# Performance work log

Hardware: AMD Instinct MI355X
Metric: run time of the kernel (lower is better)

Reference implementation:

```python
import jax, jax.numpy as jnp
import numpy as np

L = 12        # depth
DIM = 768     # model dim
HEADS = 12
DHEAD = 64
INNER = HEADS * DHEAD   # 768
MLP = 3072
P = 16        # patch size
IMG = 384
C = 3
B = 16
NCLS = 1000
NPATCH = (IMG // P) ** 2   # 576
N = NPATCH + 1             # 577 (cls token)
PATCH_DIM = C * P * P      # 768
SCALE = DIM ** (-0.5)      # NOTE: original scales by dim, not dim_head


def setup_inputs() -> dict:
    key = jax.random.key(0)
    ks = jax.random.split(key, 21)
    rn = lambda k, shape, s=0.02: jax.random.normal(k, shape, dtype=jnp.float32) * s
    return {
        "img": jax.random.normal(ks[0], (B, C, IMG, IMG), dtype=jnp.float32),
        "patch_w": rn(ks[1], (PATCH_DIM, DIM)),
        "patch_b": rn(ks[2], (DIM,)),
        "pos_emb": rn(ks[3], (1, N, DIM), 1.0),
        "cls_tok": rn(ks[4], (1, 1, DIM), 1.0),
        "ln1_w": jnp.ones((L, DIM), jnp.float32),
        "ln1_b": jnp.zeros((L, DIM), jnp.float32),
        "qkv_w": rn(ks[5], (L, DIM, 3 * INNER)),
        "out_w": rn(ks[6], (L, INNER, DIM)),
        "out_b": rn(ks[7], (L, DIM)),
        "ln2_w": jnp.ones((L, DIM), jnp.float32),
        "ln2_b": jnp.zeros((L, DIM), jnp.float32),
        "ff1_w": rn(ks[8], (L, DIM, MLP)),
        "ff1_b": rn(ks[9], (L, MLP)),
        "ff2_w": rn(ks[10], (L, MLP, DIM)),
        "ff2_b": rn(ks[11], (L, DIM)),
        "head_ln_w": jnp.ones((DIM,), jnp.float32),
        "head_ln_b": jnp.zeros((DIM,), jnp.float32),
        "head_w": rn(ks[12], (DIM, NCLS)),
        "head_b": rn(ks[13], (NCLS,)),
    }


def layer_norm(x, w, b, eps=1e-5):
    mu = jnp.mean(x, axis=-1, keepdims=True)
    var = jnp.mean(jnp.square(x - mu), axis=-1, keepdims=True)
    return (x - mu) * jax.lax.rsqrt(var + eps) * w + b


def _vit_forward(img, patch_w, patch_b, pos_emb, cls_tok,
                 ln1_w, ln1_b, qkv_w, out_w, out_b,
                 ln2_w, ln2_b, ff1_w, ff1_b, ff2_w, ff2_b,
                 head_ln_w, head_ln_b, head_w, head_b):
    b = img.shape[0]
    g = IMG // P
    # rearrange 'b c (h p1) (w p2) -> b (h w) (p1 p2 c)'
    x = img.reshape(b, C, g, P, g, P).transpose(0, 2, 4, 3, 5, 1).reshape(b, NPATCH, PATCH_DIM)
    x = x @ patch_w + patch_b                           # [b, 576, dim]
    cls = jnp.broadcast_to(cls_tok, (b, 1, DIM))
    x = jnp.concatenate([cls, x], axis=1) + pos_emb[:, :N]   # [b, 577, dim]

    def block(x, p):
        l1w, l1b, qkvw, ow, ob, l2w, l2b, f1w, f1b, f2w, f2b = p
        # attention (pre-norm, residual inside Attention.forward)
        h = layer_norm(x, l1w, l1b)
        qkv = h @ qkvw                                  # [b, n, 3*inner]
        q, k, v = jnp.split(qkv, 3, axis=-1)
        to_heads = lambda t: t.reshape(b, N, HEADS, DHEAD).transpose(0, 2, 1, 3)
        q, k, v = to_heads(q), to_heads(k), to_heads(v)  # [b, h, n, d]
        dots = jnp.einsum('bhid,bhjd->bhij', q, k) * SCALE
        attn = jax.nn.softmax(dots, axis=-1)
        o = jnp.einsum('bhij,bhjd->bhid', attn, v)
        o = o.transpose(0, 2, 1, 3).reshape(b, N, INNER)
        x = x + (o @ ow + ob)
        # feedforward (pre-norm, residual)
        h2 = layer_norm(x, l2w, l2b)
        h2 = jax.nn.gelu(h2 @ f1w + f1b, approximate=False)
        x = x + (h2 @ f2w + f2b)
        return x, None

    x, _ = jax.lax.scan(block, x,
                        (ln1_w, ln1_b, qkv_w, out_w, out_b,
                         ln2_w, ln2_b, ff1_w, ff1_b, ff2_w, ff2_b))
    cls_out = x[:, 0]                                   # [b, dim]
    return layer_norm(cls_out, head_ln_w, head_ln_b) @ head_w + head_b


def reference(img, patch_w, patch_b, pos_emb, cls_tok,
              ln1_w, ln1_b, qkv_w, out_w, out_b,
              ln2_w, ln2_b, ff1_w, ff1_b, ff2_w, ff2_b,
              head_ln_w, head_ln_b, head_w, head_b):
    return _vit_forward(img, patch_w, patch_b, pos_emb, cls_tok,
                        ln1_w, ln1_b, qkv_w, out_w, out_b,
                        ln2_w, ln2_b, ff1_w, ff1_b, ff2_w, ff2_b,
                        head_ln_w, head_ln_b, head_w, head_b)
```

## Files before the change

### kernel.cpp

```cpp
#include <hip/hip_runtime.h>
#include <cstdint>


typedef __attribute__((ext_vector_type(8))) short bf16x8;
typedef __attribute__((ext_vector_type(4))) float f32x4;

#define NTOK 577

__device__ __forceinline__ ushort f2bf(float f) {
  union { float f; unsigned int u; } x; x.f = f;
  unsigned int r = x.u + 0x7fffu + ((x.u >> 16) & 1u);
  return (ushort)(r >> 16);
}

__device__ __forceinline__ void gload_lds16(const ushort* g, ushort* l) {
  __builtin_amdgcn_global_load_lds(
      (const __attribute__((address_space(1))) unsigned int*)g,
      (__attribute__((address_space(3))) unsigned int*)l, 16, 0, 0);
}

#define VMCNT0 asm volatile("s_waitcnt vmcnt(0)" ::: "memory")
#define LGKM0  asm volatile("s_waitcnt lgkmcnt(0)" ::: "memory")
#define SCHED0 __builtin_amdgcn_sched_barrier(0)
#define BARRIER __builtin_amdgcn_s_barrier()

__device__ __forceinline__ int gsw(int row) {
  return (row & 7) + 2 * ((row >> 4) & 3);
}

__global__ __launch_bounds__(256) void convt_kernel(const float* __restrict__ W,
                                                    ushort* __restrict__ Wt,
                                                    int K, int N) {
  __shared__ float t[32][33];
  const int kb = blockIdx.x * 32, nb = blockIdx.y * 32;
  const int tx = threadIdx.x & 31, ty = threadIdx.x >> 5;
#pragma unroll
  for (int i = 0; i < 32; i += 8)
    t[ty + i][tx] = W[(size_t)(kb + ty + i) * N + (nb + tx)];
  __syncthreads();
#pragma unroll
  for (int i = 0; i < 32; i += 8)
    Wt[(size_t)(nb + ty + i) * K + (kb + tx)] = f2bf(t[tx][ty + i]);
}

__global__ __launch_bounds__(256) void im2col_kernel(const float* __restrict__ img,
                                                     ushort* __restrict__ Ap) {
  const int idx = blockIdx.x * 256 + threadIdx.x;
  const int j = idx % 768;
  const int m = idx / 768;
  const int c = j % 3;
  const int q = j / 3;
  const int px = q & 15, py = q >> 4;
  const int b = m / 576, p = m % 576;
  const int gy = p / 24, gx = p % 24;
  const float v = img[((size_t)(b * 3 + c) * 384 + (gy * 16 + py)) * 384 + (gx * 16 + px)];
  Ap[idx] = f2bf(v);
}

__global__ void clspos_kernel(const float* __restrict__ cls_tok,
                              const float* __restrict__ pos,
                              float* __restrict__ x) {
  const int i = blockIdx.x * 256 + threadIdx.x;
  const int b = i / 768, d = i % 768;
  x[(size_t)b * NTOK * 768 + d] = cls_tok[d] + pos[d];
}

__global__ __launch_bounds__(64) void ln_kernel(const float* __restrict__ x,
                                                const float* __restrict__ w,
                                                const float* __restrict__ bb,
                                                ushort* __restrict__ out) {
  const int row = blockIdx.x, lane = threadIdx.x;
  const float4* xr = reinterpret_cast<const float4*>(x + (size_t)row * 768);
  const float4 v0 = xr[lane], v1 = xr[lane + 64], v2 = xr[lane + 128];
  float vals[12] = {v0.x, v0.y, v0.z, v0.w, v1.x, v1.y, v1.z, v1.w,
                    v2.x, v2.y, v2.z, v2.w};
  float s = 0.f;
#pragma unroll
  for (int i = 0; i < 12; ++i) s += vals[i];
#pragma unroll
  for (int o = 32; o; o >>= 1) s += __shfl_xor(s, o);
  const float mu = s * (1.0f / 768.0f);
  float q = 0.f;
#pragma unroll
  for (int i = 0; i < 12; ++i) { const float d = vals[i] - mu; q += d * d; }
#pragma unroll
  for (int o = 32; o; o >>= 1) q += __shfl_xor(q, o);
  const float rstd = rsqrtf(q * (1.0f / 768.0f) + 1e-5f);
  const float4* w4 = reinterpret_cast<const float4*>(w);
  const float4* b4 = reinterpret_cast<const float4*>(bb);
  ushort* orow = out + (size_t)row * 768;
#pragma unroll
  for (int ch = 0; ch < 3; ++ch) {
    const float4 wv = w4[lane + ch * 64];
    const float4 bv = b4[lane + ch * 64];
    ushort4 u;
    u.x = f2bf((vals[ch * 4 + 0] - mu) * rstd * wv.x + bv.x);
    u.y = f2bf((vals[ch * 4 + 1] - mu) * rstd * wv.y + bv.y);
    u.z = f2bf((vals[ch * 4 + 2] - mu) * rstd * wv.z + bv.z);
    u.w = f2bf((vals[ch * 4 + 3] - mu) * rstd * wv.w + bv.w);
    *reinterpret_cast<ushort4*>(orow + ch * 256 + lane * 4) = u;
  }
}

constexpr int EPI_BF16 = 0;
constexpr int EPI_GELU_BF16 = 1;
constexpr int EPI_RES_F32 = 2;
constexpr int EPI_PATCH = 3;

template <int EPI>
__global__ __launch_bounds__(256) void gemmP_kernel(
    const ushort* __restrict__ A, const ushort* __restrict__ Bt,
    const float* __restrict__ bias, const float* __restrict__ extra,
    void* __restrict__ Cptr, int M, int N, int K, int mt) {
  __shared__ ushort ldsA[2][128 * 64];
  __shared__ ushort ldsB[2][128 * 64];

  const int nwg = gridDim.x;
  const int orig = blockIdx.x;
  const int q8 = nwg >> 3, r8 = nwg & 7, xcd = orig & 7, sidx = orig >> 3;
  const int wg = (xcd < r8 ? xcd * (q8 + 1) : r8 * (q8 + 1) + (xcd - r8) * q8) + sidx;
  const int tileM = (wg % mt) * 128;
  const int tileN = (wg / mt) * 128;

  const int tid = threadIdx.x;
  const int wave = tid >> 6, lane = tid & 63;
  const int wm = wave >> 1, wn = wave & 1;
  const int lr = lane & 15, lg = lane >> 4;

  f32x4 acc[4][4];
#pragma unroll
  for (int m = 0; m < 4; ++m)
#pragma unroll
    for (int n = 0; n < 4; ++n) acc[m][n] = (f32x4){0.f, 0.f, 0.f, 0.f};

  const ushort* pA[4];
  const ushort* pB[4];
  int dst[4];
#pragma unroll
  for (int i = 0; i < 4; ++i) {
    const int c = wave * 4 + i;
    const int rowst = c * 8;
    dst[i] = rowst * 64;
    const int row = rowst + (lane >> 3);
    const int lgr = ((lane & 7) - gsw(row)) & 7;
    pA[i] = A + (size_t)(tileM + row) * K + lgr * 8;
    pB[i] = Bt + (size_t)(tileN + row) * K + lgr * 8;
  }

#define PSTAGE(buf, kk)                              \
  _Pragma("unroll") for (int i = 0; i < 4; ++i)      \
      gload_lds16(pA[i] + (kk), &ldsA[buf][dst[i]]); \
  _Pragma("unroll") for (int i = 0; i < 4; ++i)      \
      gload_lds16(pB[i] + (kk), &ldsB[buf][dst[i]]);

  PSTAGE(0, 0);

  const int NT = K >> 6;
  int cb = 0;
  for (int t = 0; t < NT; ++t) {
    VMCNT0; SCHED0;
    BARRIER;
    if (t + 1 < NT) { PSTAGE(cb ^ 1, (t + 1) * 64); }
    bf16x8 a[8], b[8];
#pragma unroll
    for (int mf = 0; mf < 4; ++mf) {
      const int row = wm * 64 + mf * 16 + lr;
#pragma unroll
      for (int ks = 0; ks < 2; ++ks) {
        const int pg = (ks * 4 + lg + (lr & 7) + 2 * mf) & 7;
        a[mf * 2 + ks] = *reinterpret_cast<const bf16x8*>(&ldsA[cb][row * 64 + pg * 8]);
      }
    }
#pragma unroll
    for (int nf = 0; nf < 4; ++nf) {
      const int row = wn * 64 + nf * 16 + lr;
#pragma unroll
      for (int ks = 0; ks < 2; ++ks) {
        const int pg = (ks * 4 + lg + (lr & 7) + 2 * nf) & 7;
        b[nf * 2 + ks] = *reinterpret_cast<const bf16x8*>(&ldsB[cb][row * 64 + pg * 8]);
      }
    }
    LGKM0; SCHED0;
    __builtin_amdgcn_s_setprio(1);
#pragma unroll
    for (int mf = 0; mf < 4; ++mf)
#pragma unroll
      for (int nf = 0; nf < 4; ++nf)
#pragma unroll
        for (int ks = 0; ks < 2; ++ks)
          acc[mf][nf] = __builtin_amdgcn_mfma_f32_16x16x32_bf16(
              a[mf * 2 + ks], b[nf * 2 + ks], acc[mf][nf], 0, 0, 0);
    __builtin_amdgcn_s_setprio(0);
    cb ^= 1;
  }

#pragma unroll
  for (int mf = 0; mf < 4; ++mf) {
#pragma unroll
    for (int r = 0; r < 4; ++r) {
      const int row = tileM + wm * 64 + mf * 16 + lg * 4 + r;
      if (row >= M) continue;
#pragma unroll
      for (int nf = 0; nf < 4; ++nf) {
        const int col = tileN + wn * 64 + nf * 16 + lr;
        float v = acc[mf][nf][r];
        if constexpr (EPI == EPI_BF16) {
          reinterpret_cast<ushort*>(Cptr)[(size_t)row * N + col] = f2bf(v);
        } else if constexpr (EPI == EPI_GELU_BF16) {
          v += bias[col];
          v = 0.5f * v * (1.0f + erff(v * 0.70710678118654752440f));
          reinterpret_cast<ushort*>(Cptr)[(size_t)row * N + col] = f2bf(v);
        } else if constexpr (EPI == EPI_RES_F32) {
          v += bias[col] + extra[(size_t)row * N + col];
          reinterpret_cast<float*>(Cptr)[(size_t)row * N + col] = v;
        } else {
          const int bb = row / 576;
          const int p = row - bb * 576;
          v += bias[col] + extra[(size_t)(p + 1) * 768 + col];
          reinterpret_cast<float*>(Cptr)[(size_t)(row + bb + 1) * 768 + col] = v;
        }
      }
    }
  }
#undef PSTAGE
}

__global__ __launch_bounds__(256) void attn_kernel(const ushort* __restrict__ qkv,
                                                   ushort* __restrict__ o) {
  __shared__ ushort sK[64 * 64];
  __shared__ ushort sVt[64 * 64];
  __shared__ ushort sP[4][16 * 72];
  const int bh = blockIdx.x;
  const int b = bh / 12, hh = bh % 12;
  const int q0 = blockIdx.y * 64;
  const int tid = threadIdx.x;
  const int wave = tid >> 6, lane = tid & 63;
  const int lr = lane & 15;
  const int lg = lane >> 4;
  const ushort* base = qkv + (size_t)b * NTOK * 2304 + hh * 64;
  const float SC = 0.03608439182435161f;

  bf16x8 qf[2];
  {
    const int qrow = q0 + wave * 16 + lr;
    if (qrow < NTOK) {
      const ushort* qp = base + (size_t)qrow * 2304 + lg * 8;
      qf[0] = *reinterpret_cast<const bf16x8*>(qp);
      qf[1] = *reinterpret_cast<const bf16x8*>(qp + 32);
    } else {
      qf[0] = (bf16x8){0, 0, 0, 0, 0, 0, 0, 0};
      qf[1] = qf[0];
    }
  }

  float mst[4], lst[4];
  f32x4 oacc[4];
#pragma unroll
  for (int i = 0; i < 4; ++i) {
    mst[i] = -1e30f; lst[i] = 0.f;
    oacc[i] = (f32x4){0.f, 0.f, 0.f, 0.f};
  }

  const int skey = tid >> 2;
  const int sc4 = tid & 3;
  const int gswk = gsw(skey);

  for (int t0 = 0; t0 < NTOK; t0 += 64) {
    __syncthreads();
    {
      const int gk = t0 + skey;
      int4 k0v, k1v, v0v, v1v;
      if (gk < NTOK) {
        const int4* kp = reinterpret_cast<const int4*>(base + (size_t)gk * 2304 + 768 + sc4 * 16);
        k0v = kp[0]; k1v = kp[1];
        const int4* vp = reinterpret_cast<const int4*>(base + (size_t)gk * 2304 + 1536 + sc4 * 16);
        v0v = vp[0]; v1v = vp[1];
      } else {
        int4 z; z.x = z.y = z.z = z.w = 0;
        k0v = k1v = v0v = v1v = z;
      }
      *reinterpret_cast<int4*>(&sK[skey * 64 + (((2 * sc4 + 0) + gswk) & 7) * 8]) = k0v;
      *reinterpret_cast<int4*>(&sK[skey * 64 + (((2 * sc4 + 1) + gswk) & 7) * 8]) = k1v;
      const ushort* vs = reinterpret_cast<const ushort*>(&v0v);
      const ushort* vs2 = reinterpret_cast<const ushort*>(&v1v);
#pragma unroll
      for (int i = 0; i < 8; ++i) {
        const int d0 = sc4 * 16 + i;
        const int pg0 = ((skey >> 3) + gsw(d0)) & 7;
        sVt[d0 * 64 + pg0 * 8 + (skey & 7)] = vs[i];
        const int d1 = sc4 * 16 + 8 + i;
        const int pg1 = ((skey >> 3) + gsw(d1)) & 7;
        sVt[d1 * 64 + pg1 * 8 + (skey & 7)] = vs2[i];
      }
    }
    __syncthreads();

    f32x4 sacc[4];
#pragma unroll
    for (int n = 0; n < 4; ++n) sacc[n] = (f32x4){0.f, 0.f, 0.f, 0.f};
#pragma unroll
    for (int n = 0; n < 4; ++n) {
      const int row = n * 16 + lr;
      const int rot = (lr & 7) + 2 * n;
      const bf16x8 kf0 = *reinterpret_cast<const bf16x8*>(&sK[row * 64 + ((lg + rot) & 7) * 8]);
      const bf16x8 kf1 = *reinterpret_cast<const bf16x8*>(&sK[row * 64 + ((4 + lg + rot) & 7) * 8]);
      sacc[n] = __builtin_amdgcn_mfma_f32_16x16x32_bf16(qf[0], kf0, sacc[n], 0, 0, 0);
      sacc[n] = __builtin_amdgcn_mfma_f32_16x16x32_bf16(qf[1], kf1, sacc[n], 0, 0, 0);
    }

    float s[4][4], pm[4];
#pragma unroll
    for (int reg = 0; reg < 4; ++reg) pm[reg] = -1e30f;
#pragma unroll
    for (int n = 0; n < 4; ++n)
#pragma unroll
      for (int reg = 0; reg < 4; ++reg) {
        float v = sacc[n][reg] * SC;
        if (t0 + n * 16 + lr >= NTOK) v = -1e30f;
        s[n][reg] = v;
        pm[reg] = fmaxf(pm[reg], v);
      }
#pragma unroll
    for (int off = 1; off < 16; off <<= 1)
#pragma unroll
      for (int reg = 0; reg < 4; ++reg) pm[reg] = fmaxf(pm[reg], __shfl_xor(pm[reg], off));

    float al[4], rs[4];
#pragma unroll
    for (int reg = 0; reg < 4; ++reg) {
      const float mn = fmaxf(mst[reg], pm[reg]);
      al[reg] = __expf(mst[reg] - mn);
      mst[reg] = mn;
      rs[reg] = 0.f;
    }
#pragma unroll
    for (int n = 0; n < 4; ++n)
#pragma unroll
      for (int reg = 0; reg < 4; ++reg) {
        s[n][reg] = __expf(s[n][reg] - mst[reg]);
        rs[reg] += s[n][reg];
      }
#pragma unroll
    for (int off = 1; off < 16; off <<= 1)
#pragma unroll
      for (int reg = 0; reg < 4; ++reg) rs[reg] += __shfl_xor(rs[reg], off);
#pragma unroll
    for (int reg = 0; reg < 4; ++reg) {
      lst[reg] = lst[reg] * al[reg] + rs[reg];
#pragma unroll
      for (int n = 0; n < 4; ++n) oacc[n][reg] *= al[reg];
    }

#pragma unroll
    for (int n = 0; n < 4; ++n)
#pragma unroll
      for (int reg = 0; reg < 4; ++reg)
        sP[wave][(lg * 4 + reg) * 72 + n * 16 + lr] = f2bf(s[n][reg]);

    const bf16x8 pf0 = *reinterpret_cast<const bf16x8*>(&sP[wave][lr * 72 + lg * 8]);
    const bf16x8 pf1 = *reinterpret_cast<const bf16x8*>(&sP[wave][lr * 72 + 32 + lg * 8]);
#pragma unroll
    for (int n = 0; n < 4; ++n) {
      const int row = n * 16 + lr;
      const int rot = (lr & 7) + 2 * n;
      const bf16x8 vf0 = *reinterpret_cast<const bf16x8*>(&sVt[row * 64 + ((lg + rot) & 7) * 8]);
      const bf16x8 vf1 = *reinterpret_cast<const bf16x8*>(&sVt[row * 64 + ((4 + lg + rot) & 7) * 8]);
      oacc[n] = __builtin_amdgcn_mfma_f32_16x16x32_bf16(pf0, vf0, oacc[n], 0, 0, 0);
      oacc[n] = __builtin_amdgcn_mfma_f32_16x16x32_bf16(pf1, vf1, oacc[n], 0, 0, 0);
    }
  }

#pragma unroll
  for (int reg = 0; reg < 4; ++reg) {
    const int q = q0 + wave * 16 + lg * 4 + reg;
    if (q >= NTOK) continue;
    const float inv = 1.0f / lst[reg];
    ushort* op = o + (size_t)(b * NTOK + q) * 768 + hh * 64;
#pragma unroll
    for (int n = 0; n < 4; ++n) op[n * 16 + lr] = f2bf(oacc[n][reg] * inv);
  }
}

__global__ __launch_bounds__(256) void head_kernel(const float* __restrict__ x,
                                                   const float* __restrict__ lw,
                                                   const float* __restrict__ lb,
                                                   const float* __restrict__ hw,
                                                   const float* __restrict__ hb,
                                                   float* __restrict__ out) {
  __shared__ float srow[768];
  __shared__ float sred[8];
  const int b = blockIdx.x, tid = threadIdx.x;
  const float* xr = x + (size_t)b * NTOK * 768;
  for (int i = tid; i < 768; i += 256) srow[i] = xr[i];
  __syncthreads();
  float part = srow[tid] + srow[tid + 256] + srow[tid + 512];
#pragma unroll
  for (int off = 32; off; off >>= 1) part += __shfl_xor(part, off);
  if ((tid & 63) == 0) sred[tid >> 6] = part;
  __syncthreads();
  const float mu = (sred[0] + sred[1] + sred[2] + sred[3]) * (1.0f / 768.0f);
  const float d0 = srow[tid] - mu, d1 = srow[tid + 256] - mu, d2 = srow[tid + 512] - mu;
  float vp = d0 * d0 + d1 * d1 + d2 * d2;
#pragma unroll
  for (int off = 32; off; off >>= 1) vp += __shfl_xor(vp, off);
  if ((tid & 63) == 0) sred[4 + (tid >> 6)] = vp;
  __syncthreads();
  const float rstd = rsqrtf((sred[4] + sred[5] + sred[6] + sred[7]) * (1.0f / 768.0f) + 1e-5f);
  for (int i = tid; i < 768; i += 256) srow[i] = (srow[i] - mu) * rstd * lw[i] + lb[i];
  __syncthreads();
  const int c = blockIdx.y * 250 + tid;
  if (tid < 250 && c < 1000) {
    float a = 0.f;
#pragma unroll 4
    for (int k = 0; k < 768; ++k) a += srow[k] * hw[(size_t)k * 1000 + c];
    out[b * 1000 + c] = a + hb[c];
  }
}

extern "C" void kernel_launch(void* const* d_in, const int* in_sizes, int n_in,
                              void* d_out, int out_size, void* d_ws, size_t ws_size,
                              hipStream_t stream) {
  const float* img     = (const float*)d_in[0];
  const float* patch_w = (const float*)d_in[1];
  const float* patch_b = (const float*)d_in[2];
  const float* pos_emb = (const float*)d_in[3];
  const float* cls_tok = (const float*)d_in[4];
  const float* ln1_w   = (const float*)d_in[5];
  const float* ln1_b   = (const float*)d_in[6];
  const float* qkv_w   = (const float*)d_in[7];
  const float* out_w   = (const float*)d_in[8];
  const float* out_b   = (const float*)d_in[9];
  const float* ln2_w   = (const float*)d_in[10];
  const float* ln2_b   = (const float*)d_in[11];
  const float* ff1_w   = (const float*)d_in[12];
  const float* ff1_b   = (const float*)d_in[13];
  const float* ff2_w   = (const float*)d_in[14];
  const float* ff2_b   = (const float*)d_in[15];
  const float* hln_w   = (const float*)d_in[16];
  const float* hln_b   = (const float*)d_in[17];
  const float* head_w  = (const float*)d_in[18];
  const float* head_b  = (const float*)d_in[19];
  float* outp = (float*)d_out;

  char* wsp = (char*)d_ws;
  auto alloc = [&](size_t bytes) {
    char* p = wsp;
    wsp += (bytes + 255) & ~(size_t)255;
    return p;
  };
  float*  x    = (float*) alloc((size_t)9232 * 768 * 4);
  ushort* h    = (ushort*)alloc((size_t)9232 * 768 * 2);
  ushort* qkvb = (ushort*)alloc((size_t)9232 * 2304 * 2);
  ushort* mlp  = (ushort*)alloc((size_t)9232 * 3072 * 2);
  ushort* wq   = (ushort*)alloc((size_t)768 * 2304 * 2);
  ushort* wo   = (ushort*)alloc((size_t)768 * 768 * 2);
  ushort* w1   = (ushort*)alloc((size_t)768 * 3072 * 2);
  ushort* w2   = (ushort*)alloc((size_t)3072 * 768 * 2);
  ushort* apatch = mlp;
  ushort* wpatch = wq;

  convt_kernel<<<dim3(24, 24), 256, 0, stream>>>(patch_w, wpatch, 768, 768);
  im2col_kernel<<<27648, 256, 0, stream>>>(img, apatch);
  gemmP_kernel<EPI_PATCH><<<72 * 6, 256, 0, stream>>>(
      apatch, wpatch, patch_b, pos_emb, x, 9216, 768, 768, 72);
  clspos_kernel<<<48, 256, 0, stream>>>(cls_tok, pos_emb, x);

  for (int l = 0; l < 12; ++l) {
    ln_kernel<<<9232, 64, 0, stream>>>(x, ln1_w + l * 768, ln1_b + l * 768, h);
    convt_kernel<<<dim3(24, 72), 256, 0, stream>>>(qkv_w + (size_t)l * 768 * 2304, wq, 768, 2304);
    gemmP_kernel<EPI_BF16><<<73 * 18, 256, 0, stream>>>(
        h, wq, nullptr, nullptr, qkvb, 9232, 2304, 768, 73);
    attn_kernel<<<dim3(192, 10), 256, 0, stream>>>(qkvb, h);
    convt_kernel<<<dim3(24, 24), 256, 0, stream>>>(out_w + (size_t)l * 768 * 768, wo, 768, 768);
    gemmP_kernel<EPI_RES_F32><<<73 * 6, 256, 0, stream>>>(
        h, wo, out_b + l * 768, x, x, 9232, 768, 768, 73);
    ln_kernel<<<9232, 64, 0, stream>>>(x, ln2_w + l * 768, ln2_b + l * 768, h);
    convt_kernel<<<dim3(24, 96), 256, 0, stream>>>(ff1_w + (size_t)l * 768 * 3072, w1, 768, 3072);
    gemmP_kernel<EPI_GELU_BF16><<<73 * 24, 256, 0, stream>>>(
        h, w1, ff1_b + l * 3072, nullptr, mlp, 9232, 3072, 768, 73);
    convt_kernel<<<dim3(96, 24), 256, 0, stream>>>(ff2_w + (size_t)l * 3072 * 768, w2, 3072, 768);
    gemmP_kernel<EPI_RES_F32><<<73 * 6, 256, 0, stream>>>(
        mlp, w2, ff2_b + l * 768, x, x, 9232, 768, 3072, 73);
  }

  head_kernel<<<dim3(16, 4), 256, 0, stream>>>(x, hln_w, hln_b, head_w, head_b, outp);
}
```

Before: 4.485 ms.

## Batch weight conversions, pack LN rows, prefetch attention KV, reorder GEMM tiles

Merges the four per-layer weight transpose/convert launches into one kernel, so there is one launch per layer instead of four. LayerNorm now processes four rows per 256-thread block instead of one row per 64-thread block. Attention software-prefetches the next K/V tile into registers while the current tile is computed. The QKV and FF1 GEMMs switch to N-fastest tile ordering, which may improve L2 reuse of A tiles. The head kernel splits K across waves and uses more blocks.

```diff
diff --git a/kernel.cpp b/kernel.cpp
--- a/kernel.cpp
+++ b/kernel.cpp
@@ -28,19 +28,47 @@
   return (row & 7) + 2 * ((row >> 4) & 3);
 }
 
+__device__ __forceinline__ void transpose_tile(const float* __restrict__ W,
+                                               ushort* __restrict__ Wt,
+                                               int K, int N, int kb, int nb,
+                                               int tx, int ty, float t[32][33]) {
+#pragma unroll
+  for (int i = 0; i < 32; i += 8)
+    t[ty + i][tx] = W[(size_t)(kb + ty + i) * N + (nb + tx)];
+  __syncthreads();
+#pragma unroll
+  for (int i = 0; i < 32; i += 8)
+    Wt[(size_t)(nb + ty + i) * K + (kb + tx)] = f2bf(t[tx][ty + i]);
+}
+
 __global__ __launch_bounds__(256) void convt_kernel(const float* __restrict__ W,
                                                     ushort* __restrict__ Wt,
                                                     int K, int N) {
   __shared__ float t[32][33];
-  const int kb = blockIdx.x * 32, nb = blockIdx.y * 32;
+  transpose_tile(W, Wt, K, N, blockIdx.x * 32, blockIdx.y * 32,
+                 threadIdx.x & 31, threadIdx.x >> 5, t);
+}
+
+__global__ __launch_bounds__(256) void wconv_kernel(
+    const float* __restrict__ qkv_w, const float* __restrict__ out_w,
+    const float* __restrict__ ff1_w, const float* __restrict__ ff2_w,
+    ushort* __restrict__ wq, ushort* __restrict__ wo,
+    ushort* __restrict__ w1, ushort* __restrict__ w2) {
+  __shared__ float t[32][33];
   const int tx = threadIdx.x & 31, ty = threadIdx.x >> 5;
-#pragma unroll
-  for (int i = 0; i < 32; i += 8)
-    t[ty + i][tx] = W[(size_t)(kb + ty + i) * N + (nb + tx)];
-  __syncthreads();
-#pragma unroll
-  for (int i = 0; i < 32; i += 8)
-    Wt[(size_t)(nb + ty + i) * K + (kb + tx)] = f2bf(t[tx][ty + i]);
+  int bx = blockIdx.x;
+  if (bx < 1728) {
+    transpose_tile(qkv_w, wq, 768, 2304, (bx % 24) * 32, (bx / 24) * 32, tx, ty, t);
+  } else if (bx < 2304) {
+    bx -= 1728;
+    transpose_tile(out_w, wo, 768, 768, (bx % 24) * 32, (bx / 24) * 32, tx, ty, t);
+  } else if (bx < 4608) {
+    bx -= 2304;
+    transpose_tile(ff1_w, w1, 768, 3072, (bx % 24) * 32, (bx / 24) * 32, tx, ty, t);
+  } else {
+    bx -= 4608;
+    transpose_tile(ff2_w, w2, 3072, 768, (bx % 96) * 32, (bx / 96) * 32, tx, ty, t);
+  }
 }
 
 __global__ __launch_bounds__(256) void im2col_kernel(const float* __restrict__ img,
@@ -65,11 +93,12 @@
   x[(size_t)b * NTOK * 768 + d] = cls_tok[d] + pos[d];
 }
 
-__global__ __launch_bounds__(64) void ln_kernel(const float* __restrict__ x,
-                                                const float* __restrict__ w,
-                                                const float* __restrict__ bb,
-                                                ushort* __restrict__ out) {
-  const int row = blockIdx.x, lane = threadIdx.x;
+__global__ __launch_bounds__(256) void ln_kernel(const float* __restrict__ x,
+                                                 const float* __restrict__ w,
+                                                 const float* __restrict__ bb,
+                                                 ushort* __restrict__ out) {
+  const int wave = threadIdx.x >> 6, lane = threadIdx.x & 63;
+  const int row = blockIdx.x * 4 + wave;
   const float4* xr = reinterpret_cast<const float4*>(x + (size_t)row * 768);
   const float4 v0 = xr[lane], v1 = xr[lane + 64], v2 = xr[lane + 128];
   float vals[12] = {v0.x, v0.y, v0.z, v0.w, v1.x, v1.y, v1.z, v1.w,
@@ -107,7 +136,7 @@
 constexpr int EPI_RES_F32 = 2;
 constexpr int EPI_PATCH = 3;
 
-template <int EPI>
+template <int EPI, bool NFAST>
 __global__ __launch_bounds__(256) void gemmP_kernel(
     const ushort* __restrict__ A, const ushort* __restrict__ Bt,
     const float* __restrict__ bias, const float* __restrict__ extra,
@@ -119,8 +148,14 @@
   const int orig = blockIdx.x;
   const int q8 = nwg >> 3, r8 = nwg & 7, xcd = orig & 7, sidx = orig >> 3;
   const int wg = (xcd < r8 ? xcd * (q8 + 1) : r8 * (q8 + 1) + (xcd - r8) * q8) + sidx;
-  const int tileM = (wg % mt) * 128;
-  const int tileN = (wg / mt) * 128;
+  int tileM, tileN;
+  if (NFAST) {
+    tileM = (wg / mt) * 128;
+    tileN = (wg % mt) * 128;
+  } else {
+    tileM = (wg % mt) * 128;
+    tileN = (wg / mt) * 128;
+  }
 
   const int tid = threadIdx.x;
   const int wave = tid >> 6, lane = tid & 63;
@@ -265,20 +300,24 @@
   const int sc4 = tid & 3;
   const int gswk = gsw(skey);
 
+  int4 k0v, k1v, v0v, v1v;
+  auto load_kv = [&](int t0) {
+    const int gk = t0 + skey;
+    if (gk < NTOK) {
+      const int4* kp = reinterpret_cast<const int4*>(base + (size_t)gk * 2304 + 768 + sc4 * 16);
+      k0v = kp[0]; k1v = kp[1];
+      const int4* vp = reinterpret_cast<const int4*>(base + (size_t)gk * 2304 + 1536 + sc4 * 16);
+      v0v = vp[0]; v1v = vp[1];
+    } else {
+      int4 z; z.x = z.y = z.z = z.w = 0;
+      k0v = k1v = v0v = v1v = z;
+    }
+  };
+  load_kv(0);
+
   for (int t0 = 0; t0 < NTOK; t0 += 64) {
     __syncthreads();
     {
-      const int gk = t0 + skey;
-      int4 k0v, k1v, v0v, v1v;
-      if (gk < NTOK) {
-        const int4* kp = reinterpret_cast<const int4*>(base + (size_t)gk * 2304 + 768 + sc4 * 16);
-        k0v = kp[0]; k1v = kp[1];
-        const int4* vp = reinterpret_cast<const int4*>(base + (size_t)gk * 2304 + 1536 + sc4 * 16);
-        v0v = vp[0]; v1v = vp[1];
-      } else {
-        int4 z; z.x = z.y = z.z = z.w = 0;
-        k0v = k1v = v0v = v1v = z;
-      }
       *reinterpret_cast<int4*>(&sK[skey * 64 + (((2 * sc4 + 0) + gswk) & 7) * 8]) = k0v;
       *reinterpret_cast<int4*>(&sK[skey * 64 + (((2 * sc4 + 1) + gswk) & 7) * 8]) = k1v;
       const ushort* vs = reinterpret_cast<const ushort*>(&v0v);
@@ -295,6 +334,8 @@
     }
     __syncthreads();
 
+    if (t0 + 64 < NTOK) load_kv(t0 + 64);
+
     f32x4 sacc[4];
 #pragma unroll
     for (int n = 0; n < 4; ++n) sacc[n] = (f32x4){0.f, 0.f, 0.f, 0.f};
@@ -389,7 +430,8 @@
                                                    float* __restrict__ out) {
   __shared__ float srow[768];
   __shared__ float sred[8];
-  const int b = blockIdx.x, tid = threadIdx.x;
+  __shared__ float spart[4][64];
+  const int b = blockIdx.x, ct = blockIdx.y, tid = threadIdx.x;
   const float* xr = x + (size_t)b * NTOK * 768;
   for (int i = tid; i < 768; i += 256) srow[i] = xr[i];
   __syncthreads();
@@ -408,12 +450,21 @@
   const float rstd = rsqrtf((sred[4] + sred[5] + sred[6] + sred[7]) * (1.0f / 768.0f) + 1e-5f);
   for (int i = tid; i < 768; i += 256) srow[i] = (srow[i] - mu) * rstd * lw[i] + lb[i];
   __syncthreads();
-  const int c = blockIdx.y * 250 + tid;
-  if (tid < 250 && c < 1000) {
-    float a = 0.f;
-#pragma unroll 4
-    for (int k = 0; k < 768; ++k) a += srow[k] * hw[(size_t)k * 1000 + c];
-    out[b * 1000 + c] = a + hb[c];
+  const int cl = tid & 63, kq = tid >> 6;
+  const int c = ct * 64 + cl;
+  float a = 0.f;
+  if (c < 1000) {
+    const int k0 = kq * 192;
+#pragma unroll 8
+    for (int k = k0; k < k0 + 192; ++k) a += srow[k] * hw[(size_t)k * 1000 + c];
+  }
+  spart[kq][cl] = a;
+  __syncthreads();
+  if (tid < 64) {
+    const int c2 = ct * 64 + tid;
+    if (c2 < 1000)
+      out[b * 1000 + c2] =
+          spart[0][tid] + spart[1][tid] + spart[2][tid] + spart[3][tid] + hb[c2];
   }
 }
 
@@ -461,27 +512,27 @@
 
   convt_kernel<<<dim3(24, 24), 256, 0, stream>>>(patch_w, wpatch, 768, 768);
   im2col_kernel<<<27648, 256, 0, stream>>>(img, apatch);
-  gemmP_kernel<EPI_PATCH><<<72 * 6, 256, 0, stream>>>(
+  gemmP_kernel<EPI_PATCH, false><<<72 * 6, 256, 0, stream>>>(
       apatch, wpatch, patch_b, pos_emb, x, 9216, 768, 768, 72);
   clspos_kernel<<<48, 256, 0, stream>>>(cls_tok, pos_emb, x);
 
   for (int l = 0; l < 12; ++l) {
-    ln_kernel<<<9232, 64, 0, stream>>>(x, ln1_w + l * 768, ln1_b + l * 768, h);
-    convt_kernel<<<dim3(24, 72), 256, 0, stream>>>(qkv_w + (size_t)l * 768 * 2304, wq, 768, 2304);
-    gemmP_kernel<EPI_BF16><<<73 * 18, 256, 0, stream>>>(
-        h, wq, nullptr, nullptr, qkvb, 9232, 2304, 768, 73);
+    wconv_kernel<<<6912, 256, 0, stream>>>(
+        qkv_w + (size_t)l * 768 * 2304, out_w + (size_t)l * 768 * 768,
+        ff1_w + (size_t)l * 768 * 3072, ff2_w + (size_t)l * 3072 * 768,
+        wq, wo, w1, w2);
+    ln_kernel<<<2308, 256, 0, stream>>>(x, ln1_w + l * 768, ln1_b + l * 768, h);
+    gemmP_kernel<EPI_BF16, true><<<73 * 18, 256, 0, stream>>>(
+        h, wq, nullptr, nullptr, qkvb, 9232, 2304, 768, 18);
     attn_kernel<<<dim3(192, 10), 256, 0, stream>>>(qkvb, h);
-    convt_kernel<<<dim3(24, 24), 256, 0, stream>>>(out_w + (size_t)l * 768 * 768, wo, 768, 768);
-    gemmP_kernel<EPI_RES_F32><<<73 * 6, 256, 0, stream>>>(
+    gemmP_kernel<EPI_RES_F32, false><<<73 * 6, 256, 0, stream>>>(
         h, wo, out_b + l * 768, x, x, 9232, 768, 768, 73);
-    ln_kernel<<<9232, 64, 0, stream>>>(x, ln2_w + l * 768, ln2_b + l * 768, h);
-    convt_kernel<<<dim3(24, 96), 256, 0, stream>>>(ff1_w + (size_t)l * 768 * 3072, w1, 768, 3072);
-    gemmP_kernel<EPI_GELU_BF16><<<73 * 24, 256, 0, stream>>>(
-        h, w1, ff1_b + l * 3072, nullptr, mlp, 9232, 3072, 768, 73);
-    convt_kernel<<<dim3(96, 24), 256, 0, stream>>>(ff2_w + (size_t)l * 3072 * 768, w2, 3072, 768);
-    gemmP_kernel<EPI_RES_F32><<<73 * 6, 256, 0, stream>>>(
+    ln_kernel<<<2308, 256, 0, stream>>>(x, ln2_w + l * 768, ln2_b + l * 768, h);
+    gemmP_kernel<EPI_GELU_BF16, true><<<73 * 24, 256, 0, stream>>>(
+        h, w1, ff1_b + l * 3072, nullptr, mlp, 9232, 3072, 768, 24);
+    gemmP_kernel<EPI_RES_F32, false><<<73 * 6, 256, 0, stream>>>(
         mlp, w2, ff2_b + l * 768, x, x, 9232, 768, 3072, 73);
   }
 
-  head_kernel<<<dim3(16, 4), 256, 0, stream>>>(x, hln_w, hln_b, head_w, head_b, outp);
-}
+  head_kernel<<<dim3(16, 16), 256, 0, stream>>>(x, hln_w, hln_b, head_w, head_b, outp);
+}
```

Result: no change. 4.444 ms (-0.9%).
